# Kernel tuning notes

Hardware: AMD Instinct MI355X
Metric: run time of the kernel (lower is better)

## Reference

```python
import jax, jax.numpy as jnp
import numpy as np

E = 8_388_608  # total edges across batched graphs
G = 4096       # num_graphs


def setup_inputs() -> dict:
    key = jax.random.key(0)
    k1, k2, k3 = jax.random.split(key, 3)
    edge_scores = jax.random.normal(k1, (E,), dtype=jnp.float32)
    # edge_batch: sorted segment ids in [0, G), as in PyG batched graphs
    edge_batch = jnp.sort(jax.random.randint(k2, (E,), 0, G)).astype(jnp.int32)
    candidate_mask = jax.random.bernoulli(k3, 0.5, (E,))
    return {
        "edge_scores": edge_scores,
        "edge_batch": edge_batch,
        "candidate_mask": candidate_mask,
        "num_graphs": G,
        "k": 32,
    }


def reference(edge_scores, edge_batch, candidate_mask, num_graphs, k):
    """Segmented top-k edge selection (GFlowNetActor._select_topk_candidate_edges).

    Faithful fixed-shape formulation: candidate edges come in as a boolean mask
    over all E edges (the rollout builds cand_edges = nonzero(candidate_mask)),
    and the kept top-k-per-graph edges go out as a boolean pruned mask (the
    rollout scatters the returned indices back into pruned_mask). Also returns
    the score values gated by the pruned mask (differentiable output).
    """
    n = edge_scores.shape[0]
    neg_inf = jnp.finfo(jnp.float32).min
    # Non-candidates get -inf so they sort to the back of each segment
    s = jnp.where(candidate_mask, edge_scores.astype(jnp.float32), neg_inf)
    # Sort by score descending, then stably by segment id -> within each
    # graph edges appear in descending-score order (same double-argsort as torch)
    order_score = jnp.argsort(-s, stable=True)
    order_seg = jnp.argsort(edge_batch[order_score], stable=True)
    perm = order_score[order_seg]          # [E] edge ids sorted by (seg asc, score desc)
    seg_sorted = edge_batch[perm]          # [E]
    # Segment starts via bincount + exclusive cumsum
    counts = jnp.bincount(seg_sorted, length=num_graphs)
    start = jnp.concatenate(
        [jnp.zeros(1, jnp.int32), jnp.cumsum(counts)[:-1].astype(jnp.int32)]
    )
    rank = jnp.arange(n, dtype=jnp.int32) - start[seg_sorted]
    keep_sorted = (rank < k) & candidate_mask[perm]
    # Scatter keep flags back to original edge order
    pruned_mask = jnp.zeros(n, dtype=bool).at[perm].set(keep_sorted)
    pruned_scores = jnp.where(pruned_mask, edge_scores, jnp.float32(0.0))
    return pruned_mask, pruned_scores
```

## Files before the change

### kernel.cpp

```cpp
#include <hip/hip_runtime.h>
#include <stdint.h>

#define G_NUM 4096
#define BLOCK 128
#define VPT   24
#define NCH   (VPT / 4)
#define CAP   (BLOCK * VPT - 3)
#define CLS   256
#define HB    1024
#define NW    (BLOCK / 64)

typedef unsigned long long ull;

__device__ __forceinline__ unsigned int order_bits(float f) {
    unsigned int b = __float_as_uint(f);
    return (b & 0x80000000u) ? ~b : (b | 0x80000000u);
}
__device__ __forceinline__ float inv_order_bits(unsigned int ob) {
    return __uint_as_float((ob & 0x80000000u) ? (ob & 0x7FFFFFFFu) : ~ob);
}

__global__ void prep_kernel(const int* __restrict__ batch, int* __restrict__ start,
                            const unsigned int* __restrict__ mraw, int* __restrict__ flag,
                            int E) {
    if (blockIdx.x == 0 && threadIdx.x < 64) {
        int lane = threadIdx.x;
        bool allI = true, allF = true;
        for (int i = lane; i < 256; i += 64) {
            unsigned int w = mraw[i];
            if (w > 1u) allI = false;
            if (w != 0u && w != 0x3F800000u) allF = false;
        }
        allI = __all(allI);
        allF = __all(allF);
        if (lane == 0) *flag = allI ? 0 : (allF ? 1 : 2);
    }
    int t = blockIdx.x * blockDim.x + threadIdx.x;
    if (t > G_NUM) return;
    if (t == G_NUM) { start[G_NUM] = E; return; }
    int lo = 0, hi = E;
    while (lo < hi) {
        int mid = (lo + hi) >> 1;
        if (batch[mid] < t) lo = mid + 1; else hi = mid;
    }
    start[t] = lo;
}

template <int NPT>
__device__ __forceinline__ void scan_sel(
    unsigned int* hist, unsigned int* wtot, int kk,
    int* bsel_s, unsigned int* cgt_s, unsigned int* hsel_s, int* cnt2, int tid)
{
    unsigned int h[NPT];
    unsigned int S = 0u;
    const int b0 = tid * NPT;
    #pragma unroll
    for (int j = 0; j < NPT; ++j) { h[j] = hist[b0 + j]; S += h[j]; hist[b0 + j] = 0u; }
    unsigned int v = S;
    int lane = tid & 63, wv = tid >> 6;
    #pragma unroll
    for (int off = 1; off < 64; off <<= 1) {
        unsigned int o = __shfl_down(v, off, 64);
        if (lane + off < 64) v += o;
    }
    if (lane == 0) wtot[wv] = v;
    if (tid == 0) *cnt2 = 0;
    __syncthreads();
    unsigned int sfx = v;
    for (int w = wv + 1; w < NW; ++w) sfx += wtot[w];
    unsigned int run = sfx - S;
    #pragma unroll
    for (int j = NPT - 1; j >= 0; --j) {
        unsigned int inc = run + h[j];
        if ((unsigned)kk <= inc && (unsigned)kk > run) {
            *bsel_s = b0 + j; *cgt_s = run; *hsel_s = h[j];
        }
        run = inc;
    }
    __syncthreads();
}

__global__ __launch_bounds__(BLOCK) void topk_kernel(
    const float* __restrict__ scores, const void* __restrict__ maskp,
    const int* __restrict__ start, const int* __restrict__ kp,
    const int* __restrict__ flagp, float* __restrict__ out_mask,
    float* __restrict__ out_scores, int E)
{
    __shared__ unsigned int hist[HB];
    __shared__ unsigned int wtot[NW];
    __shared__ ull cls[CLS];
    __shared__ int cnt, cnt2, bsel_s, licut_s;
    __shared__ unsigned int cgt_s, hsel_s, P_s;

    const int g  = blockIdx.x;
    const int s0 = start[g];
    const int s1 = start[g + 1];
    const int len = s1 - s0;
    if (len <= 0) return;

    const int k     = *kp;
    const int mflag = *flagp;
    const int tid   = threadIdx.x;

    auto getmask = [&](int i) -> bool {
        if (mflag == 2) return ((const unsigned char*)maskp)[i] != 0;
        if (mflag == 0) return ((const int*)maskp)[i] != 0;
        return ((const float*)maskp)[i] != 0.0f;
    };

    if (k <= 0) {
        for (int i = s0 + tid; i < s1; i += BLOCK) { out_mask[i] = 0.0f; out_scores[i] = 0.0f; }
        return;
    }

    #pragma unroll
    for (int j = 0; j < HB / BLOCK; ++j) hist[tid + j * BLOCK] = 0u;
    if (tid == 0) cnt = 0;

    if (len <= CAP) {
        const int a0 = s0 & ~3;
        unsigned int key[VPT];
        unsigned int candm = 0u;

        #pragma unroll
        for (int q = 0; q < NCH; ++q) {
            const int g0 = a0 + 4 * (q * BLOCK + tid);
            if (g0 >= s0 && g0 + 4 <= s1) {
                float4 f = *(const float4*)(scores + g0);
                key[4*q]   = order_bits(f.x);
                key[4*q+1] = order_bits(f.y);
                key[4*q+2] = order_bits(f.z);
                key[4*q+3] = order_bits(f.w);
                unsigned int cm4 = 0u;
                if (mflag == 2) {
                    unsigned int w = *(const unsigned int*)((const unsigned char*)maskp + g0);
                    #pragma unroll
                    for (int j = 0; j < 4; ++j)
                        if ((w >> (8*j)) & 0xFFu) cm4 |= 1u << j;
                } else if (mflag == 0) {
                    int4 w = *(const int4*)((const int*)maskp + g0);
                    if (w.x) cm4 |= 1u; if (w.y) cm4 |= 2u;
                    if (w.z) cm4 |= 4u; if (w.w) cm4 |= 8u;
                } else {
                    float4 w = *(const float4*)((const float*)maskp + g0);
                    if (w.x != 0.0f) cm4 |= 1u; if (w.y != 0.0f) cm4 |= 2u;
                    if (w.z != 0.0f) cm4 |= 4u; if (w.w != 0.0f) cm4 |= 8u;
                }
                candm |= cm4 << (4*q);
            } else if (g0 < s1) {
                #pragma unroll
                for (int j = 0; j < 4; ++j) {
                    int gi = g0 + j;
                    key[4*q+j] = 0u;
                    if (gi >= s0 && gi < s1) {
                        key[4*q+j] = order_bits(scores[gi]);
                        if (getmask(gi)) candm |= 1u << (4*q+j);
                    }
                }
            } else {
                #pragma unroll
                for (int j = 0; j < 4; ++j) key[4*q+j] = 0u;
            }
        }

        __syncthreads();
        #pragma unroll
        for (int v = 0; v < VPT; ++v)
            if ((candm >> v) & 1u) atomicAdd(&hist[key[v] >> 22], 1u);
        int lc = __popc(candm);
        #pragma unroll
        for (int off = 1; off < 64; off <<= 1) lc += __shfl_xor(lc, off, 64);
        if ((tid & 63) == 0) atomicAdd(&cnt, lc);
        __syncthreads();
        const int m = cnt;
        const bool keep_all = (m <= k);
        unsigned int P = 0u;
        int licut = 0;

        if (!keep_all) {
            int kk = k;
            scan_sel<HB / BLOCK>(hist, wtot, kk, &bsel_s, &cgt_s, &hsel_s, &cnt2, tid);
            unsigned int prefix = ((unsigned int)bsel_s) << 22;
            kk -= (int)cgt_s;
            int csel = (int)hsel_s;
            int low  = 22;

            if (csel > CLS) {
                const int lows[3]   = {14, 6, 0};
                const int widths[3] = {8, 8, 6};
                for (int r = 0; r < 3; ++r) {
                    const int lw = lows[r], wd = widths[r];
                    const unsigned int dm = (1u << wd) - 1u;
                    #pragma unroll
                    for (int v = 0; v < VPT; ++v)
                        if (((candm >> v) & 1u) &&
                            ((key[v] >> (lw + wd)) == (prefix >> (lw + wd))))
                            atomicAdd(&hist[(key[v] >> lw) & dm], 1u);
                    __syncthreads();
                    scan_sel<256 / BLOCK>(hist, wtot, kk, &bsel_s, &cgt_s, &hsel_s, &cnt2, tid);
                    prefix |= ((unsigned int)bsel_s) << lw;
                    kk  -= (int)cgt_s;
                    csel = (int)hsel_s;
                    low  = lw;
                    if (csel <= CLS) break;
                }
            }

            if (csel <= CLS) {
                const int dl = a0 - s0;
                #pragma unroll
                for (int v = 0; v < VPT; ++v) {
                    if (((candm >> v) & 1u) && ((key[v] >> low) == (prefix >> low))) {
                        int q = v >> 2;
                        int li = dl + 4 * (q * BLOCK + tid) + (v & 3);
                        cls[atomicAdd(&cnt2, 1)] = ((ull)key[v] << 32) | (unsigned int)li;
                    }
                }
                __syncthreads();
                for (int e = tid; e < csel; e += BLOCK) {
                    ull me = cls[e];
                    unsigned int km = (unsigned int)(me >> 32), lm = (unsigned int)me;
                    int r = 0;
                    for (int j = 0; j < csel; ++j) {
                        ull o = cls[j];
                        unsigned int ko = (unsigned int)(o >> 32), lo = (unsigned int)o;
                        r += (ko > km || (ko == km && lo < lm)) ? 1 : 0;
                    }
                    if (r == kk - 1) { P_s = km; licut_s = (int)lm; }
                }
                __syncthreads();
                P = P_s; licut = licut_s;
            } else {
                P = prefix;
                const int dl = a0 - s0;
                int lo = 0, hi = len - 1;
                while (lo < hi) {
                    int mid = (lo + hi) >> 1;
                    if (tid == 0) cnt2 = 0;
                    __syncthreads();
                    int c = 0;
                    #pragma unroll
                    for (int v = 0; v < VPT; ++v) {
                        int q = v >> 2;
                        int li = dl + 4 * (q * BLOCK + tid) + (v & 3);
                        if (((candm >> v) & 1u) && key[v] == prefix && li <= mid) c++;
                    }
                    #pragma unroll
                    for (int off = 1; off < 64; off <<= 1) c += __shfl_xor(c, off, 64);
                    if ((tid & 63) == 0) atomicAdd(&cnt2, c);
                    __syncthreads();
                    int total = cnt2;
                    __syncthreads();
                    if (total >= kk) hi = mid; else lo = mid + 1;
                }
                licut = lo;
            }
        }

        const int dl = a0 - s0;
        #pragma unroll
        for (int q = 0; q < NCH; ++q) {
            const int g0 = a0 + 4 * (q * BLOCK + tid);
            if (g0 >= s0 && g0 + 4 <= s1) {
                float4 vm, vs;
                float* pm = (float*)&vm;
                float* ps = (float*)&vs;
                #pragma unroll
                for (int j = 0; j < 4; ++j) {
                    int v = 4*q + j;
                    int li = dl + 4 * (q * BLOCK + tid) + j;
                    bool kept = ((candm >> v) & 1u) &&
                        (keep_all || key[v] > P || (key[v] == P && li <= licut));
                    pm[j] = kept ? 1.0f : 0.0f;
                    ps[j] = kept ? inv_order_bits(key[v]) : 0.0f;
                }
                *(float4*)(out_mask   + g0) = vm;
                *(float4*)(out_scores + g0) = vs;
            } else if (g0 < s1) {
                #pragma unroll
                for (int j = 0; j < 4; ++j) {
                    int gi = g0 + j;
                    if (gi < s0 || gi >= s1) continue;
                    int v = 4*q + j;
                    int li = gi - s0;
                    bool kept = ((candm >> v) & 1u) &&
                        (keep_all || key[v] > P || (key[v] == P && li <= licut));
                    out_mask[gi]   = kept ? 1.0f : 0.0f;
                    out_scores[gi] = kept ? inv_order_bits(key[v]) : 0.0f;
                }
            }
        }
    } else {
        __syncthreads();
        int lc = 0;
        for (int i = s0 + tid; i < s1; i += BLOCK)
            if (getmask(i)) lc++;
        atomicAdd(&cnt, lc);
        __syncthreads();
        const int m = cnt;
        const bool keep_all = (m <= k);
        ull pivot = 0ull;
        if (!keep_all) {
            ull prefix = 0ull;
            int kk = k;
            for (int shift = 56; shift >= 0; shift -= 8) {
                for (int i = s0 + tid; i < s1; i += BLOCK) {
                    if (!getmask(i)) continue;
                    ull key = ((ull)order_bits(scores[i]) << 32) |
                              (ull)(0xFFFFFFFFu - (unsigned)(i - s0));
                    if (shift == 56 || (key >> (shift + 8)) == (prefix >> (shift + 8)))
                        atomicAdd(&hist[(unsigned)((key >> shift) & 0xFFull)], 1u);
                }
                __syncthreads();
                scan_sel<256 / BLOCK>(hist, wtot, kk, &bsel_s, &cgt_s, &hsel_s, &cnt2, tid);
                prefix |= ((ull)(unsigned)bsel_s) << shift;
                kk -= (int)cgt_s;
            }
            pivot = prefix;
        }
        for (int i = s0 + tid; i < s1; i += BLOCK) {
            bool c = getmask(i);
            float sc = 0.0f;
            bool kept = false;
            if (c) {
                sc = scores[i];
                ull key = ((ull)order_bits(sc) << 32) |
                          (ull)(0xFFFFFFFFu - (unsigned)(i - s0));
                kept = keep_all || (key >= pivot);
            }
            out_mask[i]   = kept ? 1.0f : 0.0f;
            out_scores[i] = kept ? sc : 0.0f;
        }
    }
}

extern "C" void kernel_launch(void* const* d_in, const int* in_sizes, int n_in,
                              void* d_out, int out_size, void* d_ws, size_t ws_size,
                              hipStream_t stream) {
    const float* scores = (const float*)d_in[0];
    const int*   batch  = (const int*)d_in[1];
    const void*  mask   = d_in[2];
    const int*   kp     = (const int*)d_in[4];
    const int    E      = in_sizes[0];

    float* out_mask   = (float*)d_out;
    float* out_scores = out_mask + E;

    int* flag  = (int*)d_ws;
    int* start = (int*)((char*)d_ws + 256);

    prep_kernel<<<(G_NUM + 1 + BLOCK - 1) / BLOCK, BLOCK, 0, stream>>>(
        batch, start, (const unsigned int*)mask, flag, E);
    topk_kernel<<<G_NUM, BLOCK, 0, stream>>>(scores, mask, start, kp, flag,
                                             out_mask, out_scores, E);
}
```

Before: 49.55 us.

## Assign one wavefront per graph with barrier-free wave-level radix select

Each graph segment is now processed by a single 64-lane wavefront instead of a 128-thread block, with four graphs per 256-thread block. Block-wide __syncthreads and the shared counters are replaced by wave shuffles, ballots and lgkmcnt waits. Keys are compacted to 16-bit prefixes in LDS for the candidate-collection pass, and inputs are re-read from global memory on each pass instead of being held in registers. This removes block barriers and lets the hardware hide latency across more independent segments. In exchange, per-graph work is serialized over fewer lanes, there are extra global reloads, the float-mask path is dropped, and correctness now depends on the wave-level LDS ordering assumptions holding.

```diff
diff --git a/kernel.cpp b/kernel.cpp
--- a/kernel.cpp
+++ b/kernel.cpp
@@ -2,15 +2,18 @@
 #include <stdint.h>
 
 #define G_NUM 4096
-#define BLOCK 128
-#define VPT   24
-#define NCH   (VPT / 4)
-#define CAP   (BLOCK * VPT - 3)
-#define CLS   256
-#define HB    1024
-#define NW    (BLOCK / 64)
+#define BLOCK 256
+#define WPB   4
+#define CAP   3069
+#define KCAP  3072
+#define HB    512
+#define CLS   384
 
 typedef unsigned long long ull;
+
+__device__ __forceinline__ void wsync() {
+    asm volatile("s_waitcnt lgkmcnt(0)" ::: "memory");
+}
 
 __device__ __forceinline__ unsigned int order_bits(float f) {
     unsigned int b = __float_as_uint(f);
@@ -47,37 +50,33 @@
 }
 
 template <int NPT>
-__device__ __forceinline__ void scan_sel(
-    unsigned int* hist, unsigned int* wtot, int kk,
-    int* bsel_s, unsigned int* cgt_s, unsigned int* hsel_s, int* cnt2, int tid)
+__device__ __forceinline__ void wave_sel(unsigned int* hist, int lane, int kk,
+                                         int& bsel, unsigned int& cgt, unsigned int& csel)
 {
     unsigned int h[NPT];
     unsigned int S = 0u;
-    const int b0 = tid * NPT;
+    const int b0 = lane * NPT;
     #pragma unroll
     for (int j = 0; j < NPT; ++j) { h[j] = hist[b0 + j]; S += h[j]; hist[b0 + j] = 0u; }
     unsigned int v = S;
-    int lane = tid & 63, wv = tid >> 6;
     #pragma unroll
     for (int off = 1; off < 64; off <<= 1) {
         unsigned int o = __shfl_down(v, off, 64);
         if (lane + off < 64) v += o;
     }
-    if (lane == 0) wtot[wv] = v;
-    if (tid == 0) *cnt2 = 0;
-    __syncthreads();
-    unsigned int sfx = v;
-    for (int w = wv + 1; w < NW; ++w) sfx += wtot[w];
-    unsigned int run = sfx - S;
+    unsigned int run = v - S;
+    int fj = -1; unsigned int fc = 0u, fs = 0u;
     #pragma unroll
     for (int j = NPT - 1; j >= 0; --j) {
         unsigned int inc = run + h[j];
-        if ((unsigned)kk <= inc && (unsigned)kk > run) {
-            *bsel_s = b0 + j; *cgt_s = run; *hsel_s = h[j];
-        }
+        if (fj < 0 && (unsigned)kk <= inc && (unsigned)kk > run) { fj = j; fc = run; fs = h[j]; }
         run = inc;
     }
-    __syncthreads();
+    ull bm = __ballot(fj >= 0);
+    int wl = (int)(__ffsll((long long)bm) - 1);
+    bsel = __shfl(b0 + fj, wl);
+    cgt  = __shfl(fc, wl);
+    csel = __shfl(fs, wl);
 }
 
 __global__ __launch_bounds__(BLOCK) void topk_kernel(
@@ -86,13 +85,14 @@
     const int* __restrict__ flagp, float* __restrict__ out_mask,
     float* __restrict__ out_scores, int E)
 {
-    __shared__ unsigned int hist[HB];
-    __shared__ unsigned int wtot[NW];
-    __shared__ ull cls[CLS];
-    __shared__ int cnt, cnt2, bsel_s, licut_s;
-    __shared__ unsigned int cgt_s, hsel_s, P_s;
-
-    const int g  = blockIdx.x;
+    __shared__ unsigned short k16s[WPB][KCAP];
+    __shared__ unsigned int   hists[WPB][HB];
+
+    const int tid  = threadIdx.x;
+    const int lane = tid & 63;
+    const int w    = tid >> 6;
+    const int g    = blockIdx.x * WPB + w;
+
     const int s0 = start[g];
     const int s1 = start[g + 1];
     const int len = s1 - s0;
@@ -100,179 +100,177 @@
 
     const int k     = *kp;
     const int mflag = *flagp;
-    const int tid   = threadIdx.x;
+    unsigned short* k16 = k16s[w];
+    unsigned int*  hist = hists[w];
 
     auto getmask = [&](int i) -> bool {
         if (mflag == 2) return ((const unsigned char*)maskp)[i] != 0;
-        if (mflag == 0) return ((const int*)maskp)[i] != 0;
-        return ((const float*)maskp)[i] != 0.0f;
+        return ((const int*)maskp)[i] != 0;
     };
 
     if (k <= 0) {
-        for (int i = s0 + tid; i < s1; i += BLOCK) { out_mask[i] = 0.0f; out_scores[i] = 0.0f; }
+        for (int i = s0 + lane; i < s1; i += 64) { out_mask[i] = 0.0f; out_scores[i] = 0.0f; }
         return;
     }
-
-    #pragma unroll
-    for (int j = 0; j < HB / BLOCK; ++j) hist[tid + j * BLOCK] = 0u;
-    if (tid == 0) cnt = 0;
 
     if (len <= CAP) {
         const int a0 = s0 & ~3;
-        unsigned int key[VPT];
-        unsigned int candm = 0u;
-
-        #pragma unroll
-        for (int q = 0; q < NCH; ++q) {
-            const int g0 = a0 + 4 * (q * BLOCK + tid);
+        const int dl = a0 - s0;
+        const int nch = (s1 - a0 + 255) >> 8;
+
+        auto load_cm4 = [&](int g0) -> unsigned int {
+            unsigned int cm4 = 0u;
+            if (mflag == 2) {
+                unsigned int mw = *(const unsigned int*)((const unsigned char*)maskp + g0);
+                if (mw & 0x000000FFu) cm4 |= 1u;
+                if (mw & 0x0000FF00u) cm4 |= 2u;
+                if (mw & 0x00FF0000u) cm4 |= 4u;
+                if (mw & 0xFF000000u) cm4 |= 8u;
+            } else {
+                int4 mw = *(const int4*)((const int*)maskp + g0);
+                if (mw.x) cm4 |= 1u; if (mw.y) cm4 |= 2u;
+                if (mw.z) cm4 |= 4u; if (mw.w) cm4 |= 8u;
+            }
+            return cm4;
+        };
+        auto load_chunk = [&](int q, unsigned int kk4[4]) -> unsigned int {
+            const int g0 = a0 + 4 * (q * 64 + lane);
+            unsigned int cm4 = 0u;
             if (g0 >= s0 && g0 + 4 <= s1) {
                 float4 f = *(const float4*)(scores + g0);
-                key[4*q]   = order_bits(f.x);
-                key[4*q+1] = order_bits(f.y);
-                key[4*q+2] = order_bits(f.z);
-                key[4*q+3] = order_bits(f.w);
-                unsigned int cm4 = 0u;
-                if (mflag == 2) {
-                    unsigned int w = *(const unsigned int*)((const unsigned char*)maskp + g0);
-                    #pragma unroll
-                    for (int j = 0; j < 4; ++j)
-                        if ((w >> (8*j)) & 0xFFu) cm4 |= 1u << j;
-                } else if (mflag == 0) {
-                    int4 w = *(const int4*)((const int*)maskp + g0);
-                    if (w.x) cm4 |= 1u; if (w.y) cm4 |= 2u;
-                    if (w.z) cm4 |= 4u; if (w.w) cm4 |= 8u;
-                } else {
-                    float4 w = *(const float4*)((const float*)maskp + g0);
-                    if (w.x != 0.0f) cm4 |= 1u; if (w.y != 0.0f) cm4 |= 2u;
-                    if (w.z != 0.0f) cm4 |= 4u; if (w.w != 0.0f) cm4 |= 8u;
-                }
-                candm |= cm4 << (4*q);
-            } else if (g0 < s1) {
+                kk4[0] = order_bits(f.x); kk4[1] = order_bits(f.y);
+                kk4[2] = order_bits(f.z); kk4[3] = order_bits(f.w);
+                cm4 = load_cm4(g0);
+            } else {
                 #pragma unroll
                 for (int j = 0; j < 4; ++j) {
-                    int gi = g0 + j;
-                    key[4*q+j] = 0u;
+                    int gi = g0 + j; kk4[j] = 0u;
                     if (gi >= s0 && gi < s1) {
-                        key[4*q+j] = order_bits(scores[gi]);
-                        if (getmask(gi)) candm |= 1u << (4*q+j);
+                        kk4[j] = order_bits(scores[gi]);
+                        if (getmask(gi)) cm4 |= 1u << j;
                     }
                 }
-            } else {
-                #pragma unroll
-                for (int j = 0; j < 4; ++j) key[4*q+j] = 0u;
-            }
-        }
-
-        __syncthreads();
+            }
+            return cm4;
+        };
+
         #pragma unroll
-        for (int v = 0; v < VPT; ++v)
-            if ((candm >> v) & 1u) atomicAdd(&hist[key[v] >> 22], 1u);
-        int lc = __popc(candm);
+        for (int j = 0; j < HB / 64; ++j) hist[lane + j * 64] = 0u;
+        wsync();
+
+        int lc = 0;
+        for (int q = 0; q < nch; ++q) {
+            unsigned int kk4[4];
+            unsigned int cm4 = load_chunk(q, kk4);
+            ushort4 hv; unsigned short* hp = (unsigned short*)&hv;
+            #pragma unroll
+            for (int j = 0; j < 4; ++j) {
+                unsigned int h = kk4[j] >> 16; h += (h == 0u);
+                bool c = (cm4 >> j) & 1u;
+                hp[j] = c ? (unsigned short)h : (unsigned short)0;
+                if (c) atomicAdd(&hist[h >> 7], 1u);
+            }
+            *(ushort4*)&k16[4 * (q * 64 + lane)] = hv;
+            lc += __popc(cm4);
+        }
         #pragma unroll
         for (int off = 1; off < 64; off <<= 1) lc += __shfl_xor(lc, off, 64);
-        if ((tid & 63) == 0) atomicAdd(&cnt, lc);
-        __syncthreads();
-        const int m = cnt;
-        const bool keep_all = (m <= k);
-        unsigned int P = 0u;
+        const int m = lc;
+        wsync();
+
+        const bool keepall = (m <= k);
+        unsigned int P32 = 0u;
         int licut = 0;
 
-        if (!keep_all) {
-            int kk = k;
-            scan_sel<HB / BLOCK>(hist, wtot, kk, &bsel_s, &cgt_s, &hsel_s, &cnt2, tid);
-            unsigned int prefix = ((unsigned int)bsel_s) << 22;
-            kk -= (int)cgt_s;
-            int csel = (int)hsel_s;
-            int low  = 22;
-
-            if (csel > CLS) {
-                const int lows[3]   = {14, 6, 0};
-                const int widths[3] = {8, 8, 6};
+        if (!keepall) {
+            int bsel; unsigned int cgt, csel;
+            wave_sel<HB / 64>(hist, lane, k, bsel, cgt, csel);
+            int kk2 = k - (int)cgt;
+
+            if (csel <= CLS) {
+                wsync();
+                const int tot = nch * 256;
+                for (int idx = lane; idx < tot; idx += 64) {
+                    unsigned int h = k16[idx];
+                    if (h != 0u && (int)(h >> 7) == bsel)
+                        hist[atomicAdd(&hist[HB - 1], 1u)] = (unsigned int)idx;
+                }
+                wsync();
+                unsigned int* kst = (unsigned int*)k16;
+                for (int e = lane; e < (int)csel; e += 64)
+                    kst[e] = order_bits(scores[a0 + (int)hist[e]]);
+                wsync();
+                bool found = false; unsigned int fP = 0u; int fL = 0;
+                for (int e = lane; e < (int)csel; e += 64) {
+                    unsigned int idx = hist[e], key = kst[e];
+                    int r = 0;
+                    for (int j = 0; j < (int)csel; ++j) {
+                        unsigned int kj = kst[j], ij = hist[j];
+                        if (kj > key || (kj == key && ij < idx)) r++;
+                    }
+                    if (r == kk2 - 1) { found = true; fP = key; fL = (int)idx + dl; }
+                }
+                ull bm = __ballot(found);
+                int wl = (int)(__ffsll((long long)bm) - 1);
+                P32 = __shfl(fP, wl); licut = __shfl(fL, wl);
+            } else {
+                unsigned int pfx = ((unsigned int)bsel) << 23;
+                const int lows[3] = {16, 8, 0};
+                const int wids[3] = {7, 8, 8};
                 for (int r = 0; r < 3; ++r) {
-                    const int lw = lows[r], wd = widths[r];
-                    const unsigned int dm = (1u << wd) - 1u;
-                    #pragma unroll
-                    for (int v = 0; v < VPT; ++v)
-                        if (((candm >> v) & 1u) &&
-                            ((key[v] >> (lw + wd)) == (prefix >> (lw + wd))))
-                            atomicAdd(&hist[(key[v] >> lw) & dm], 1u);
-                    __syncthreads();
-                    scan_sel<256 / BLOCK>(hist, wtot, kk, &bsel_s, &cgt_s, &hsel_s, &cnt2, tid);
-                    prefix |= ((unsigned int)bsel_s) << lw;
-                    kk  -= (int)cgt_s;
-                    csel = (int)hsel_s;
-                    low  = lw;
-                    if (csel <= CLS) break;
-                }
-            }
-
-            if (csel <= CLS) {
-                const int dl = a0 - s0;
-                #pragma unroll
-                for (int v = 0; v < VPT; ++v) {
-                    if (((candm >> v) & 1u) && ((key[v] >> low) == (prefix >> low))) {
-                        int q = v >> 2;
-                        int li = dl + 4 * (q * BLOCK + tid) + (v & 3);
-                        cls[atomicAdd(&cnt2, 1)] = ((ull)key[v] << 32) | (unsigned int)li;
+                    const int L = lows[r], W = wids[r];
+                    const unsigned int dm = (1u << W) - 1u;
+                    wsync();
+                    for (int q = 0; q < nch; ++q) {
+                        unsigned int kk4[4];
+                        unsigned int cm4 = load_chunk(q, kk4);
+                        #pragma unroll
+                        for (int j = 0; j < 4; ++j)
+                            if (((cm4 >> j) & 1u) && ((kk4[j] >> (L + W)) == (pfx >> (L + W))))
+                                atomicAdd(&hist[(kk4[j] >> L) & dm], 1u);
                     }
-                }
-                __syncthreads();
-                for (int e = tid; e < csel; e += BLOCK) {
-                    ull me = cls[e];
-                    unsigned int km = (unsigned int)(me >> 32), lm = (unsigned int)me;
-                    int r = 0;
-                    for (int j = 0; j < csel; ++j) {
-                        ull o = cls[j];
-                        unsigned int ko = (unsigned int)(o >> 32), lo = (unsigned int)o;
-                        r += (ko > km || (ko == km && lo < lm)) ? 1 : 0;
-                    }
-                    if (r == kk - 1) { P_s = km; licut_s = (int)lm; }
-                }
-                __syncthreads();
-                P = P_s; licut = licut_s;
-            } else {
-                P = prefix;
-                const int dl = a0 - s0;
+                    wsync();
+                    int b2; unsigned int cg2, cs2;
+                    if (W == 7) wave_sel<2>(hist, lane, kk2, b2, cg2, cs2);
+                    else        wave_sel<4>(hist, lane, kk2, b2, cg2, cs2);
+                    pfx |= ((unsigned int)b2) << L;
+                    kk2 -= (int)cg2;
+                }
+                P32 = pfx;
                 int lo = 0, hi = len - 1;
                 while (lo < hi) {
                     int mid = (lo + hi) >> 1;
-                    if (tid == 0) cnt2 = 0;
-                    __syncthreads();
                     int c = 0;
-                    #pragma unroll
-                    for (int v = 0; v < VPT; ++v) {
-                        int q = v >> 2;
-                        int li = dl + 4 * (q * BLOCK + tid) + (v & 3);
-                        if (((candm >> v) & 1u) && key[v] == prefix && li <= mid) c++;
+                    for (int q = 0; q < nch; ++q) {
+                        unsigned int kk4[4];
+                        unsigned int cm4 = load_chunk(q, kk4);
+                        const int g0 = a0 + 4 * (q * 64 + lane);
+                        #pragma unroll
+                        for (int j = 0; j < 4; ++j)
+                            if (((cm4 >> j) & 1u) && kk4[j] == P32 && (g0 + j - s0) <= mid) c++;
                     }
                     #pragma unroll
                     for (int off = 1; off < 64; off <<= 1) c += __shfl_xor(c, off, 64);
-                    if ((tid & 63) == 0) atomicAdd(&cnt2, c);
-                    __syncthreads();
-                    int total = cnt2;
-                    __syncthreads();
-                    if (total >= kk) hi = mid; else lo = mid + 1;
+                    if (c >= kk2) hi = mid; else lo = mid + 1;
                 }
                 licut = lo;
             }
         }
 
-        const int dl = a0 - s0;
-        #pragma unroll
-        for (int q = 0; q < NCH; ++q) {
-            const int g0 = a0 + 4 * (q * BLOCK + tid);
+        for (int q = 0; q < nch; ++q) {
+            const int g0 = a0 + 4 * (q * 64 + lane);
+            unsigned int kk4[4];
+            unsigned int cm4 = load_chunk(q, kk4);
             if (g0 >= s0 && g0 + 4 <= s1) {
                 float4 vm, vs;
-                float* pm = (float*)&vm;
-                float* ps = (float*)&vs;
+                float* pm = (float*)&vm; float* ps = (float*)&vs;
                 #pragma unroll
                 for (int j = 0; j < 4; ++j) {
-                    int v = 4*q + j;
-                    int li = dl + 4 * (q * BLOCK + tid) + j;
-                    bool kept = ((candm >> v) & 1u) &&
-                        (keep_all || key[v] > P || (key[v] == P && li <= licut));
+                    int li = g0 + j - s0;
+                    bool kept = ((cm4 >> j) & 1u) &&
+                        (keepall || kk4[j] > P32 || (kk4[j] == P32 && li <= licut));
                     pm[j] = kept ? 1.0f : 0.0f;
-                    ps[j] = kept ? inv_order_bits(key[v]) : 0.0f;
+                    ps[j] = kept ? inv_order_bits(kk4[j]) : 0.0f;
                 }
                 *(float4*)(out_mask   + g0) = vm;
                 *(float4*)(out_scores + g0) = vs;
@@ -281,44 +279,46 @@
                 for (int j = 0; j < 4; ++j) {
                     int gi = g0 + j;
                     if (gi < s0 || gi >= s1) continue;
-                    int v = 4*q + j;
                     int li = gi - s0;
-                    bool kept = ((candm >> v) & 1u) &&
-                        (keep_all || key[v] > P || (key[v] == P && li <= licut));
+                    bool kept = ((cm4 >> j) & 1u) &&
+                        (keepall || kk4[j] > P32 || (kk4[j] == P32 && li <= licut));
                     out_mask[gi]   = kept ? 1.0f : 0.0f;
-                    out_scores[gi] = kept ? inv_order_bits(key[v]) : 0.0f;
+                    out_scores[gi] = kept ? inv_order_bits(kk4[j]) : 0.0f;
                 }
             }
         }
     } else {
-        __syncthreads();
+        #pragma unroll
+        for (int j = 0; j < 4; ++j) hist[lane + j * 64] = 0u;
         int lc = 0;
-        for (int i = s0 + tid; i < s1; i += BLOCK)
+        for (int i = s0 + lane; i < s1; i += 64)
             if (getmask(i)) lc++;
-        atomicAdd(&cnt, lc);
-        __syncthreads();
-        const int m = cnt;
-        const bool keep_all = (m <= k);
+        #pragma unroll
+        for (int off = 1; off < 64; off <<= 1) lc += __shfl_xor(lc, off, 64);
+        const int m = lc;
+        const bool keepall = (m <= k);
         ull pivot = 0ull;
-        if (!keep_all) {
-            ull prefix = 0ull;
+        if (!keepall) {
+            ull pfx = 0ull;
             int kk = k;
             for (int shift = 56; shift >= 0; shift -= 8) {
-                for (int i = s0 + tid; i < s1; i += BLOCK) {
+                wsync();
+                for (int i = s0 + lane; i < s1; i += 64) {
                     if (!getmask(i)) continue;
                     ull key = ((ull)order_bits(scores[i]) << 32) |
                               (ull)(0xFFFFFFFFu - (unsigned)(i - s0));
-                    if (shift == 56 || (key >> (shift + 8)) == (prefix >> (shift + 8)))
+                    if (shift == 56 || (key >> (shift + 8)) == (pfx >> (shift + 8)))
                         atomicAdd(&hist[(unsigned)((key >> shift) & 0xFFull)], 1u);
                 }
-                __syncthreads();
-                scan_sel<256 / BLOCK>(hist, wtot, kk, &bsel_s, &cgt_s, &hsel_s, &cnt2, tid);
-                prefix |= ((ull)(unsigned)bsel_s) << shift;
-                kk -= (int)cgt_s;
-            }
-            pivot = prefix;
-        }
-        for (int i = s0 + tid; i < s1; i += BLOCK) {
+                wsync();
+                int b; unsigned int cg, cs;
+                wave_sel<4>(hist, lane, kk, b, cg, cs);
+                pfx |= ((ull)(unsigned)b) << shift;
+                kk -= (int)cg;
+            }
+            pivot = pfx;
+        }
+        for (int i = s0 + lane; i < s1; i += 64) {
             bool c = getmask(i);
             float sc = 0.0f;
             bool kept = false;
@@ -326,7 +326,7 @@
                 sc = scores[i];
                 ull key = ((ull)order_bits(sc) << 32) |
                           (ull)(0xFFFFFFFFu - (unsigned)(i - s0));
-                kept = keep_all || (key >= pivot);
+                kept = keepall || (key >= pivot);
             }
             out_mask[i]   = kept ? 1.0f : 0.0f;
             out_scores[i] = kept ? sc : 0.0f;
@@ -351,6 +351,6 @@
 
     prep_kernel<<<(G_NUM + 1 + BLOCK - 1) / BLOCK, BLOCK, 0, stream>>>(
         batch, start, (const unsigned int*)mask, flag, E);
-    topk_kernel<<<G_NUM, BLOCK, 0, stream>>>(scores, mask, start, kp, flag,
-                                             out_mask, out_scores, E);
-}
+    topk_kernel<<<G_NUM / WPB, BLOCK, 0, stream>>>(scores, mask, start, kp, flag,
+                                                   out_mask, out_scores, E);
+}
```

Result: slower. 101.0 us (+103.9%).
